# Performance work log

Measured on AMD Instinct MI355X. Metric: run time of the kernel, lower is better.

Reference implementation:

```python
import jax, jax.numpy as jnp
import numpy as np

STRIDES = (8, 16, 32)
BINS = 16
NC = 80
ALPHA, GAMMA = 0.25, 2.0
W_CLS, W_IOU, W_DFL = 1.0, 7.5, 1.5
B, MAX_GT = 32, 32
EPS = 1e-7


def setup_inputs() -> dict:
    key = jax.random.key(0)
    k0, k1, k2, k3, k4, k5, k6 = jax.random.split(key, 7)
    p0 = jax.random.normal(k0, (B, 4 * BINS + NC, 80, 80), dtype=jnp.float32)
    p1 = jax.random.normal(k1, (B, 4 * BINS + NC, 40, 40), dtype=jnp.float32)
    p2 = jax.random.normal(k2, (B, 4 * BINS + NC, 20, 20), dtype=jnp.float32)
    # realistic xyxy boxes inside a 640x640 image
    c = jax.random.uniform(k3, (B, MAX_GT, 2), minval=60.0, maxval=580.0)
    wh = jax.random.uniform(k4, (B, MAX_GT, 2), minval=16.0, maxval=120.0)
    gt_bboxes = jnp.concatenate([c - wh / 2, c + wh / 2], axis=-1).astype(jnp.float32)
    gt_labels = jax.random.randint(k5, (B, MAX_GT), 0, NC, dtype=jnp.int32)
    raw = jax.random.randint(k6, (B, 8400), 0, 20 * MAX_GT, dtype=jnp.int32)
    matched_gt_inds = jnp.where(raw < MAX_GT, raw, -1)
    return {"p0": p0, "p1": p1, "p2": p2, "gt_bboxes": gt_bboxes,
            "gt_labels": gt_labels, "matched_gt_inds": matched_gt_inds}


def _decode_scale(p, stride):
    # p: [B, 4*BINS + NC, H, W]
    Bp, C, H, W = p.shape
    dfl = p[:, :4 * BINS].reshape(Bp, 4, BINS, H, W)
    cls = p[:, 4 * BINS:]
    # DFL decode: expectation of softmax over bins, scaled by stride
    prob = jax.nn.softmax(dfl, axis=2)
    proj = jnp.arange(BINS, dtype=p.dtype)
    dist = jnp.einsum('bkchw,c->bkhw', prob, proj) * stride  # [B,4,H,W] in pixels
    ys, xs = jnp.meshgrid(jnp.arange(H), jnp.arange(W), indexing='ij')
    cx = ((xs.astype(p.dtype)) + 0.5) * stride
    cy = ((ys.astype(p.dtype)) + 0.5) * stride
    boxes = jnp.stack([cx - dist[:, 0], cy - dist[:, 1],
                       cx + dist[:, 2], cy + dist[:, 3]], axis=-1).reshape(Bp, H * W, 4)
    cls_logits = cls.transpose(0, 2, 3, 1).reshape(Bp, H * W, NC)
    dfl_flat = dfl.transpose(0, 3, 4, 1, 2).reshape(Bp, H * W, 4, BINS)
    grid = jnp.stack([cx, cy], axis=-1).reshape(H * W, 2)
    smap = jnp.full((H * W,), stride, dtype=p.dtype)
    return cls_logits, dfl_flat, boxes, grid, smap


def reference(p0, p1, p2, gt_bboxes, gt_labels, matched_gt_inds):
    outs = [_decode_scale(p, s) for p, s in zip((p0, p1, p2), STRIDES)]
    scores = jnp.concatenate([o[0] for o in outs], axis=1)   # [B,N,NC]
    dfl = jnp.concatenate([o[1] for o in outs], axis=1)      # [B,N,4,BINS]
    pboxes = jnp.concatenate([o[2] for o in outs], axis=1)   # [B,N,4]
    grid = jnp.concatenate([o[3] for o in outs], axis=0)     # [N,2]
    smap = jnp.concatenate([o[4] for o in outs], axis=0)     # [N]

    pos = matched_gt_inds >= 0                               # [B,N]
    idx = jnp.where(pos, matched_gt_inds, 0)
    lbl = jnp.take_along_axis(gt_labels, idx, axis=1)        # [B,N]
    posf = pos.astype(scores.dtype)
    tgt_scores = jax.nn.one_hot(lbl, NC, dtype=scores.dtype) * posf[..., None]

    # sigmoid focal loss (stable BCE-with-logits)
    prob = jax.nn.sigmoid(scores)
    ce = jnp.maximum(scores, 0) - scores * tgt_scores + jnp.log1p(jnp.exp(-jnp.abs(scores)))
    p_t = prob * tgt_scores + (1 - prob) * (1 - tgt_scores)
    alpha_t = tgt_scores * ALPHA + (1 - tgt_scores) * (1 - ALPHA)
    cls_elem = alpha_t * (1.0 - p_t) ** GAMMA * ce
    num_pos = jnp.maximum(posf.sum(), 1.0)
    loss_cls = cls_elem.sum() / num_pos

    # gather matched GT boxes per anchor
    tboxes = jnp.take_along_axis(gt_bboxes, idx[..., None], axis=1)  # [B,N,4]
    gx, gy = grid[None, :, 0], grid[None, :, 1]
    l = jnp.clip(gx - tboxes[..., 0], 0.0)
    t = jnp.clip(gy - tboxes[..., 1], 0.0)
    r = jnp.clip(tboxes[..., 2] - gx, 0.0)
    b_ = jnp.clip(tboxes[..., 3] - gy, 0.0)
    dists = jnp.stack([l, t, r, b_], axis=-1) / smap[None, :, None]   # [B,N,4]
    tb = jnp.clip(dists, 0.0, BINS - 1 - 1e-6)
    lo = jnp.floor(tb).astype(jnp.int32)
    hi = jnp.minimum(lo + 1, BINS - 1)
    a = tb - lo.astype(tb.dtype)
    # soft two-bin DFL target (vectorized form of the scatter_add loop)
    tdist = (jax.nn.one_hot(lo, BINS, dtype=dfl.dtype) * (1.0 - a)[..., None]
             + jax.nn.one_hot(hi, BINS, dtype=dfl.dtype) * a[..., None])   # [B,N,4,BINS]
    logp = jax.nn.log_softmax(dfl, axis=-1)
    dfl_elem = -(tdist * logp).sum(-1)                                # [B,N,4]
    loss_dfl = (dfl_elem * posf[..., None]).sum() / (num_pos * 4.0)

    # IoU loss on positives
    ix1 = jnp.maximum(pboxes[..., 0], tboxes[..., 0])
    iy1 = jnp.maximum(pboxes[..., 1], tboxes[..., 1])
    ix2 = jnp.minimum(pboxes[..., 2], tboxes[..., 2])
    iy2 = jnp.minimum(pboxes[..., 3], tboxes[..., 3])
    inter = jnp.clip(ix2 - ix1, 0.0) * jnp.clip(iy2 - iy1, 0.0)
    area_p = jnp.clip(pboxes[..., 2] - pboxes[..., 0], 0.0) * jnp.clip(pboxes[..., 3] - pboxes[..., 1], 0.0)
    area_t = jnp.clip(tboxes[..., 2] - tboxes[..., 0], 0.0) * jnp.clip(tboxes[..., 3] - tboxes[..., 1], 0.0)
    iou = inter / (area_p + area_t - inter + EPS)
    loss_iou = ((1.0 - iou) * posf).sum() / num_pos

    total = W_CLS * loss_cls + W_IOU * loss_iou + W_DFL * loss_dfl
    return total
```

## Files before the change

kernel.cpp:

```cpp
#include <hip/hip_runtime.h>
#include <math.h>

#define NCLS 80
#define BINS 16
#define BATCH 32
#define MAX_GT 32
#define NA 8400
#define AN (BATCH * NA)
#define NT 2100
#define NB_DFL 1050
#define NB_CLS 2560
#define NBLK (NB_DFL + NB_CLS)
#define NSLOT 64
#define ALPHA_C 0.25f
#define W_CLS 1.0
#define W_IOU 7.5
#define W_DFL 1.5
#define EPS_F 1e-7f

__device__ __forceinline__ float focal_elem(float s, float tt)
{
    float e   = __expf(-fabsf(s));
    float inv = 1.f / (1.f + e);
    float prob = (s >= 0.f) ? inv : e * inv;
    float ce  = fmaxf(s, 0.f) - s * tt + __logf(1.f + e);
    float p_t = prob * tt + (1.f - prob) * (1.f - tt);
    float alpha_t = tt * ALPHA_C + (1.f - tt) * (1.f - ALPHA_C);
    float om = 1.f - p_t;
    return alpha_t * om * om * ce;
}

__device__ __forceinline__ void block_write4(float c0, float c1, float c2, float c3,
                                             double* __restrict__ blk)
{
    #pragma unroll
    for (int o = 32; o > 0; o >>= 1) {
        c0 += __shfl_down(c0, o);
        c1 += __shfl_down(c1, o);
        c2 += __shfl_down(c2, o);
        c3 += __shfl_down(c3, o);
    }
    __shared__ float s4[4][4];
    const int wave = threadIdx.x >> 6, lane = threadIdx.x & 63;
    if (lane == 0) { s4[wave][0] = c0; s4[wave][1] = c1; s4[wave][2] = c2; s4[wave][3] = c3; }
    __syncthreads();
    if (threadIdx.x == 0) {
        double* o = blk + (size_t)blockIdx.x * 4;
        o[0] = (double)(s4[0][0] + s4[1][0] + s4[2][0] + s4[3][0]);
        o[1] = (double)(s4[0][1] + s4[1][1] + s4[2][1] + s4[3][1]);
        o[2] = (double)(s4[0][2] + s4[1][2] + s4[2][2] + s4[3][2]);
        o[3] = (double)(s4[0][3] + s4[1][3] + s4[2][3] + s4[3][3]);
    }
}

__global__ __launch_bounds__(256) void yolo_mega(
    const float* __restrict__ p0, const float* __restrict__ p1, const float* __restrict__ p2,
    const float* __restrict__ gt_bboxes, const int* __restrict__ gt_labels,
    const int* __restrict__ matched, double* __restrict__ blk)
{
    const int bid = blockIdx.x;

    if (bid < NB_DFL) {
        const int gdt = bid * 256 + (int)threadIdx.x;
        const int k   = gdt & 3;
        const int qg  = gdt >> 2;
        const int b   = qg / NT;
        const int t   = qg - b * NT;

        const float* p; int HW, off, gbase, h, w0; float stride;
        if (t < 1600)      { p = p0; HW = 6400; off = t * 4;          gbase = 0;    stride = 8.f;
                             h = t / 20;  w0 = (t - h * 20) * 4; }
        else if (t < 2000) { p = p1; HW = 1600; off = (t - 1600) * 4; gbase = 6400; stride = 16.f;
                             int u = t - 1600; h = u / 10; w0 = (u - h * 10) * 4; }
        else               { p = p2; HW = 400;  off = (t - 2000) * 4; gbase = 8000; stride = 32.f;
                             int u = t - 2000; h = u / 5;  w0 = (u - h * 5) * 4; }
        const float inv_s = 1.f / stride;
        const float cy = ((float)h + 0.5f) * stride;
        const float* pc = p + (size_t)(b * 144 + k * BINS) * HW + off;

        const int4 m4 = *(const int4*)(matched + (size_t)b * NA + gbase + off);
        const int mm[4] = {m4.x, m4.y, m4.z, m4.w};
        int lo[4]; float fr[4];
        #pragma unroll
        for (int j = 0; j < 4; ++j) {
            const int idx = (mm[j] >= 0) ? mm[j] : 0;
            const float4 tb = *(const float4*)(gt_bboxes + ((size_t)b * MAX_GT + idx) * 4);
            const float cx = ((float)(w0 + j) + 0.5f) * stride;
            float d = (k == 0) ? (cx - tb.x) : (k == 1) ? (cy - tb.y)
                    : (k == 2) ? (tb.z - cx) : (tb.w - cy);
            float tval = fminf(fmaxf(d, 0.f) * inv_s, (float)(BINS - 1) - 1e-6f);
            lo[j] = (int)tval;
            fr[j] = tval - (float)lo[j];
        }

        float mr[4], se[4], we[4];
        #pragma unroll
        for (int j = 0; j < 4; ++j) { mr[j] = -1e30f; se[j] = 0.f; we[j] = 0.f; }
        #pragma unroll
        for (int i0 = 0; i0 < BINS; i0 += 4) {
            float4 qa = *(const float4*)(pc + (size_t)(i0 + 0) * HW);
            float4 qb = *(const float4*)(pc + (size_t)(i0 + 1) * HW);
            float4 qc = *(const float4*)(pc + (size_t)(i0 + 2) * HW);
            float4 qd = *(const float4*)(pc + (size_t)(i0 + 3) * HW);
            const float r0[4] = {qa.x, qa.y, qa.z, qa.w};
            const float r1[4] = {qb.x, qb.y, qb.z, qb.w};
            const float r2[4] = {qc.x, qc.y, qc.z, qc.w};
            const float r3[4] = {qd.x, qd.y, qd.z, qd.w};
            #pragma unroll
            for (int j = 0; j < 4; ++j) {
                float v0 = r0[j], v1 = r1[j], v2 = r2[j], v3 = r3[j];
                float mx = fmaxf(fmaxf(v0, v1), fmaxf(v2, v3));
                float mn = fmaxf(mr[j], mx);
                float sc = __expf(mr[j] - mn);
                float e0 = __expf(v0 - mn), e1 = __expf(v1 - mn);
                float e2 = __expf(v2 - mn), e3 = __expf(v3 - mn);
                se[j] = se[j] * sc + ((e0 + e1) + (e2 + e3));
                we[j] = we[j] * sc + ((float)(i0    ) * e0 + (float)(i0 + 1) * e1
                                    + (float)(i0 + 2) * e2 + (float)(i0 + 3) * e3);
                mr[j] = mn;
            }
        }

        float part = 0.f;
        float pd[4];
        #pragma unroll
        for (int j = 0; j < 4; ++j) {
            pd[j] = (we[j] / se[j]) * stride;
            if (mm[j] >= 0) {
                float vlo = pc[(size_t)lo[j] * HW + j];
                float vhi = pc[(size_t)(lo[j] + 1) * HW + j];
                float lse = mr[j] + __logf(se[j]);
                part += -((1.f - fr[j]) * (vlo - lse) + fr[j] * (vhi - lse));
            }
        }

        const int lbase = ((int)threadIdx.x & 63) & ~3;
        float d0[4], d1[4], d2[4], d3[4];
        #pragma unroll
        for (int j = 0; j < 4; ++j) {
            d0[j] = __shfl(pd[j], lbase + 0);
            d1[j] = __shfl(pd[j], lbase + 1);
            d2[j] = __shfl(pd[j], lbase + 2);
            d3[j] = __shfl(pd[j], lbase + 3);
        }

        float iou_part = 0.f, cnt = 0.f, cls_corr = 0.f;
        if (k == 0) {
            #pragma unroll
            for (int j = 0; j < 4; ++j) {
                if (mm[j] >= 0) {
                    const float cx = ((float)(w0 + j) + 0.5f) * stride;
                    float px1 = cx - d0[j], py1 = cy - d1[j];
                    float px2 = cx + d2[j], py2 = cy + d3[j];
                    const float4 tb = *(const float4*)(gt_bboxes + ((size_t)b * MAX_GT + mm[j]) * 4);
                    float ix1 = fmaxf(px1, tb.x), iy1 = fmaxf(py1, tb.y);
                    float ix2 = fminf(px2, tb.z), iy2 = fminf(py2, tb.w);
                    float inter  = fmaxf(ix2 - ix1, 0.f) * fmaxf(iy2 - iy1, 0.f);
                    float area_p = fmaxf(px2 - px1, 0.f) * fmaxf(py2 - py1, 0.f);
                    float area_t = fmaxf(tb.z - tb.x, 0.f) * fmaxf(tb.w - tb.y, 0.f);
                    float iou = inter / (area_p + area_t - inter + EPS_F);
                    iou_part += 1.f - iou;
                    cnt += 1.f;
                    int lbl = gt_labels[b * MAX_GT + mm[j]];
                    float sv = *(p + (size_t)(b * 144 + 4 * BINS + lbl) * HW + off + j);
                    cls_corr += focal_elem(sv, 1.f) - focal_elem(sv, 0.f);
                }
            }
        }
        block_write4(cls_corr, iou_part, part, cnt, blk);
    } else {
        const int cbid = bid - NB_DFL;
        const int b = cbid / NCLS;
        const int c = cbid - b * NCLS;
        const size_t cls_ch = (size_t)(b * 144 + 4 * BINS + c);

        float4 q[9];
        const float* pl0 = p0 + cls_ch * 6400;
        #pragma unroll
        for (int i = 0; i < 6; ++i) {
            int off = (i * 256 + (int)threadIdx.x) * 4;
            q[i] = *(const float4*)(pl0 + off);
        }
        #pragma unroll
        for (int i = 6; i < 9; ++i) {
            int t  = i * 256 + (int)threadIdx.x;
            int tc = (t < NT) ? t : 0;
            const float* p; int HW, off;
            if (tc < 1600)      { p = p0; HW = 6400; off = tc * 4; }
            else if (tc < 2000) { p = p1; HW = 1600; off = (tc - 1600) * 4; }
            else                { p = p2; HW = 400;  off = (tc - 2000) * 4; }
            q[i] = *(const float4*)(p + cls_ch * HW + off);
        }

        float part = 0.f;
        #pragma unroll
        for (int i = 0; i < 9; ++i) {
            const bool valid = (i < 8) || (i * 256 + (int)threadIdx.x < NT);
            float sum = focal_elem(q[i].x, 0.f) + focal_elem(q[i].y, 0.f)
                      + focal_elem(q[i].z, 0.f) + focal_elem(q[i].w, 0.f);
            part += valid ? sum : 0.f;
        }
        block_write4(part, 0.f, 0.f, 0.f, blk);
    }
}

__global__ __launch_bounds__(256) void yolo_finalize_blocks(
    const double* __restrict__ blk, float* __restrict__ out)
{
    double s0 = 0.0, s1 = 0.0, s2 = 0.0, s3 = 0.0;
    for (int r = (int)threadIdx.x; r < NBLK; r += 256) {
        const double* row = blk + (size_t)r * 4;
        s0 += row[0]; s1 += row[1]; s2 += row[2]; s3 += row[3];
    }
    #pragma unroll
    for (int o = 32; o > 0; o >>= 1) {
        s0 += __shfl_down(s0, o); s1 += __shfl_down(s1, o);
        s2 += __shfl_down(s2, o); s3 += __shfl_down(s3, o);
    }
    __shared__ double sh[4][4];
    const int wave = threadIdx.x >> 6, lane = threadIdx.x & 63;
    if (lane == 0) { sh[wave][0] = s0; sh[wave][1] = s1; sh[wave][2] = s2; sh[wave][3] = s3; }
    __syncthreads();
    if (threadIdx.x == 0) {
        double c = 0, i = 0, d = 0, n = 0;
        for (int w = 0; w < 4; ++w) { c += sh[w][0]; i += sh[w][1]; d += sh[w][2]; n += sh[w][3]; }
        double np = (n < 1.0) ? 1.0 : n;
        out[0] = (float)(W_CLS * c / np + W_IOU * i / np + W_DFL * d / (np * 4.0));
    }
}

__device__ __forceinline__ void block_reduce_atomic(float val, double* __restrict__ target)
{
    __shared__ float s[4];
    __syncthreads();
    #pragma unroll
    for (int o = 32; o > 0; o >>= 1) val += __shfl_down(val, o);
    const int wave = threadIdx.x >> 6, lane = threadIdx.x & 63;
    if (lane == 0) s[wave] = val;
    __syncthreads();
    if (threadIdx.x == 0) atomicAdd(target, (double)(s[0] + s[1] + s[2] + s[3]));
}

__global__ __launch_bounds__(256) void yolo_loss_fused(
    const float* __restrict__ p0, const float* __restrict__ p1, const float* __restrict__ p2,
    const float* __restrict__ gt_bboxes, const int* __restrict__ gt_labels,
    const int* __restrict__ matched, double* __restrict__ acc)
{
    const int a = blockIdx.x * blockDim.x + threadIdx.x;
    const int b = blockIdx.y;
    const int slot = blockIdx.x & (NSLOT - 1);
    float cls_acc = 0.f, iou_acc = 0.f, dfl_acc = 0.f, pos_cnt = 0.f;
    if (a < NA) {
        const float* p; int HW, W; float stride; int off;
        if (a < 6400)      { p = p0; HW = 6400; W = 80; stride = 8.f;  off = a; }
        else if (a < 8000) { p = p1; HW = 1600; W = 40; stride = 16.f; off = a - 6400; }
        else               { p = p2; HW = 400;  W = 20; stride = 32.f; off = a - 8000; }
        const int h = off / W, w = off - h * W;
        const float cx = ((float)w + 0.5f) * stride, cy = ((float)h + 0.5f) * stride;
        const float* pb = p + ((size_t)b * 144) * (size_t)HW + (size_t)off;
        const int m = matched[(size_t)b * NA + a];
        const bool pos = (m >= 0);
        const int idx = pos ? m : 0;
        const int lbl = gt_labels[b * MAX_GT + idx];
        const float* tbp = gt_bboxes + ((size_t)b * MAX_GT + idx) * 4;
        const float tx1 = tbp[0], ty1 = tbp[1], tx2 = tbp[2], ty2 = tbp[3];
        float tdist[4] = {fmaxf(cx - tx1, 0.f) / stride, fmaxf(cy - ty1, 0.f) / stride,
                          fmaxf(tx2 - cx, 0.f) / stride, fmaxf(ty2 - cy, 0.f) / stride};
        float pdv[4]; float dfl_sum = 0.f;
        #pragma unroll
        for (int k = 0; k < 4; ++k) {
            float tv = fminf(tdist[k], (float)(BINS - 1) - 1e-6f);
            int lo = (int)floorf(tv);
            float fr = tv - (float)lo;
            const float* pcx = pb + (size_t)(k * BINS) * HW;
            float v[BINS];
            #pragma unroll
            for (int i = 0; i < BINS; ++i) v[i] = pcx[(size_t)i * HW];
            float mx = v[0];
            #pragma unroll
            for (int i = 1; i < BINS; ++i) mx = fmaxf(mx, v[i]);
            float se = 0.f, we = 0.f, vlo = 0.f, vhi = 0.f;
            #pragma unroll
            for (int i = 0; i < BINS; ++i) {
                float e = __expf(v[i] - mx);
                se += e; we += (float)i * e;
                vlo = (i == lo) ? v[i] : vlo;
                vhi = (i == lo + 1) ? v[i] : vhi;
            }
            pdv[k] = (we / se) * stride;
            if (pos) { float lse = mx + __logf(se); dfl_sum += -((1.f - fr) * (vlo - lse) + fr * (vhi - lse)); }
        }
        const float* pcls = pb + (size_t)(4 * BINS) * HW;
        #pragma unroll 4
        for (int c = 0; c < NCLS; ++c)
            cls_acc += focal_elem(pcls[(size_t)c * HW], (pos && c == lbl) ? 1.f : 0.f);
        if (pos) {
            float px1 = cx - pdv[0], py1 = cy - pdv[1], px2 = cx + pdv[2], py2 = cy + pdv[3];
            float ix1 = fmaxf(px1, tx1), iy1 = fmaxf(py1, ty1);
            float ix2 = fminf(px2, tx2), iy2 = fminf(py2, ty2);
            float inter  = fmaxf(ix2 - ix1, 0.f) * fmaxf(iy2 - iy1, 0.f);
            float area_p = fmaxf(px2 - px1, 0.f) * fmaxf(py2 - py1, 0.f);
            float area_t = fmaxf(tx2 - tx1, 0.f) * fmaxf(ty2 - ty1, 0.f);
            float iou = inter / (area_p + area_t - inter + EPS_F);
            iou_acc = 1.f - iou; dfl_acc = dfl_sum; pos_cnt = 1.f;
        }
    }
    block_reduce_atomic(cls_acc, &acc[0 * NSLOT + slot]);
    block_reduce_atomic(iou_acc, &acc[1 * NSLOT + slot]);
    block_reduce_atomic(dfl_acc, &acc[2 * NSLOT + slot]);
    block_reduce_atomic(pos_cnt, &acc[3 * NSLOT + slot]);
}

__global__ void yolo_loss_finalize(const double* __restrict__ acc, float* __restrict__ out)
{
    double s[4] = {0.0, 0.0, 0.0, 0.0};
    for (int q = 0; q < 4; ++q)
        for (int i = 0; i < NSLOT; ++i) s[q] += acc[q * NSLOT + i];
    double np = s[3] < 1.0 ? 1.0 : s[3];
    double total = W_CLS * s[0] / np + W_IOU * s[1] / np + W_DFL * s[2] / (np * 4.0);
    out[0] = (float)total;
}

extern "C" void kernel_launch(void* const* d_in, const int* in_sizes, int n_in,
                              void* d_out, int out_size, void* d_ws, size_t ws_size,
                              hipStream_t stream)
{
    const float* p0        = (const float*)d_in[0];
    const float* p1        = (const float*)d_in[1];
    const float* p2        = (const float*)d_in[2];
    const float* gt_bboxes = (const float*)d_in[3];
    const int*   gt_labels = (const int*)d_in[4];
    const int*   matched   = (const int*)d_in[5];
    float*  out = (float*)d_out;

    const size_t need = (size_t)NBLK * 4 * sizeof(double);

    if (ws_size >= need) {
        double* blk = (double*)d_ws;
        yolo_mega<<<NBLK, 256, 0, stream>>>(p0, p1, p2, gt_bboxes, gt_labels, matched, blk);
        yolo_finalize_blocks<<<1, 256, 0, stream>>>(blk, out);
    } else {
        double* acc = (double*)d_ws;
        (void)hipMemsetAsync(acc, 0, 4 * NSLOT * sizeof(double), stream);
        dim3 g((NA + 255) / 256, BATCH);
        yolo_loss_fused<<<g, 256, 0, stream>>>(p0, p1, p2, gt_bboxes, gt_labels, matched, acc);
        yolo_loss_finalize<<<1, 1, 0, stream>>>(acc, out);
    }
}
```

Measured before the change: 217.8 us.

## Grid-stride mega kernel, drop online-softmax max, specialize scales via templates

The fused loss kernel now runs on a fixed 2048-block grid. Each block loops over the 3610 virtual work units and accumulates its partials in registers, so the finalize kernel reads 2048 rows with 1024 threads. The DFL softmax drops the running-max rescaling and exponentiates the raw logits directly. Per-scale code is specialized with templates, and the negative focal term gets a simplified closed form. Target-bin computation now happens only for positive anchors. Dropping the max subtraction risks overflow for large logits, but it is safe for normal-distributed inputs. There is also a redundant pair of vlo/vhi loads.

```diff
diff --git a/kernel.cpp b/kernel.cpp
--- a/kernel.cpp
+++ b/kernel.cpp
@@ -10,7 +10,8 @@
 #define NT 2100
 #define NB_DFL 1050
 #define NB_CLS 2560
-#define NBLK (NB_DFL + NB_CLS)
+#define NVB (NB_DFL + NB_CLS)
+#define GRID 2048
 #define NSLOT 64
 #define ALPHA_C 0.25f
 #define W_CLS 1.0
@@ -28,6 +29,15 @@
     float alpha_t = tt * ALPHA_C + (1.f - tt) * (1.f - ALPHA_C);
     float om = 1.f - p_t;
     return alpha_t * om * om * ce;
+}
+
+__device__ __forceinline__ float focal0(float s)
+{
+    float e   = __expf(-fabsf(s));
+    float inv = 1.f / (1.f + e);
+    float prob = (s >= 0.f) ? inv : e * inv;
+    float sp  = fmaxf(s, 0.f) + __logf(1.f + e);
+    return 0.75f * prob * prob * sp;
 }
 
 __device__ __forceinline__ void block_write4(float c0, float c1, float c2, float c3,
@@ -53,177 +63,185 @@
     }
 }
 
+template<int HW, int SSTR, int WQ>
+__device__ __forceinline__ void dfl_scale(
+    const float* __restrict__ p, int b, int tl, int k, int gbase, int tid,
+    const float* __restrict__ gt_bboxes, const int* __restrict__ gt_labels,
+    const int* __restrict__ matched,
+    float& c_cls, float& c_iou, float& c_dfl, float& c_cnt)
+{
+    const float stride = (float)SSTR;
+    const float inv_s  = 1.f / stride;
+    const int h  = tl / WQ;
+    const int w0 = (tl - h * WQ) * 4;
+    const int off = tl * 4;
+    const float cy = ((float)h + 0.5f) * stride;
+    const float* pc = p + (size_t)(b * 144 + k * BINS) * HW + off;
+
+    const int4 m4 = *(const int4*)(matched + (size_t)b * NA + gbase + off);
+    const int mm[4] = {m4.x, m4.y, m4.z, m4.w};
+
+    float se[4] = {0.f, 0.f, 0.f, 0.f}, we[4] = {0.f, 0.f, 0.f, 0.f};
+    #pragma unroll
+    for (int i0 = 0; i0 < BINS; i0 += 4) {
+        float4 qv[4];
+        #pragma unroll
+        for (int r = 0; r < 4; ++r)
+            qv[r] = *(const float4*)(pc + (size_t)((i0 + r) * HW));
+        #pragma unroll
+        for (int r = 0; r < 4; ++r) {
+            const float wgt = (float)(i0 + r);
+            float e0 = __expf(qv[r].x), e1 = __expf(qv[r].y);
+            float e2 = __expf(qv[r].z), e3 = __expf(qv[r].w);
+            se[0] += e0; we[0] = fmaf(wgt, e0, we[0]);
+            se[1] += e1; we[1] = fmaf(wgt, e1, we[1]);
+            se[2] += e2; we[2] = fmaf(wgt, e2, we[2]);
+            se[3] += e3; we[3] = fmaf(wgt, e3, we[3]);
+        }
+    }
+
+    float pd[4];
+    #pragma unroll
+    for (int j = 0; j < 4; ++j) pd[j] = (we[j] / se[j]) * stride;
+
+    #pragma unroll
+    for (int j = 0; j < 4; ++j) {
+        if (mm[j] >= 0) {
+            const float4 tb = *(const float4*)(gt_bboxes + ((size_t)b * MAX_GT + mm[j]) * 4);
+            const float cx = ((float)(w0 + j) + 0.5f) * stride;
+            float d = (k == 0) ? (cx - tb.x) : (k == 1) ? (cy - tb.y)
+                    : (k == 2) ? (tb.z - cx) : (tb.w - cy);
+            float tval = fminf(fmaxf(d, 0.f) * inv_s, (float)(BINS - 1) - 1e-6f);
+            int   lo = (int)tval;
+            float fr = tval - (float)lo;
+            float vlo = pc[(size_t)(lo * HW) + 0];
+            float vhi = pc[(size_t)((lo + 1) * HW) + 0];
+            vlo = pc[(size_t)(lo * HW) + j];
+            vhi = pc[(size_t)((lo + 1) * HW) + j];
+            float lse = __logf(se[j]);
+            c_dfl += -((1.f - fr) * (vlo - lse) + fr * (vhi - lse));
+        }
+    }
+
+    const int lbase = (tid & 63) & ~3;
+    float d1[4], d2[4], d3[4];
+    #pragma unroll
+    for (int j = 0; j < 4; ++j) {
+        d1[j] = __shfl(pd[j], lbase + 1);
+        d2[j] = __shfl(pd[j], lbase + 2);
+        d3[j] = __shfl(pd[j], lbase + 3);
+    }
+    if (k == 0) {
+        #pragma unroll
+        for (int j = 0; j < 4; ++j) {
+            if (mm[j] >= 0) {
+                const float cx = ((float)(w0 + j) + 0.5f) * stride;
+                float px1 = cx - pd[j], py1 = cy - d1[j];
+                float px2 = cx + d2[j], py2 = cy + d3[j];
+                const float4 tb = *(const float4*)(gt_bboxes + ((size_t)b * MAX_GT + mm[j]) * 4);
+                float ix1 = fmaxf(px1, tb.x), iy1 = fmaxf(py1, tb.y);
+                float ix2 = fminf(px2, tb.z), iy2 = fminf(py2, tb.w);
+                float inter  = fmaxf(ix2 - ix1, 0.f) * fmaxf(iy2 - iy1, 0.f);
+                float area_p = fmaxf(px2 - px1, 0.f) * fmaxf(py2 - py1, 0.f);
+                float area_t = fmaxf(tb.z - tb.x, 0.f) * fmaxf(tb.w - tb.y, 0.f);
+                float iou = inter / (area_p + area_t - inter + EPS_F);
+                c_iou += 1.f - iou;
+                c_cnt += 1.f;
+                int lbl = gt_labels[b * MAX_GT + mm[j]];
+                float sv = *(p + (size_t)(b * 144 + 4 * BINS + lbl) * HW + off + j);
+                c_cls += focal_elem(sv, 1.f) - focal_elem(sv, 0.f);
+            }
+        }
+    }
+}
+
+__device__ __forceinline__ void cls_unit(int cvb, int tid,
+    const float* __restrict__ p0, const float* __restrict__ p1,
+    const float* __restrict__ p2, float& c_cls)
+{
+    const int b = cvb / NCLS;
+    const int c = cvb - b * NCLS;
+    const size_t cls_ch = (size_t)(b * 144 + 4 * BINS + c);
+
+    float4 q[9];
+    const float* pl0 = p0 + cls_ch * 6400;
+    #pragma unroll
+    for (int i = 0; i < 6; ++i) {
+        int off = (i * 256 + tid) * 4;
+        q[i] = *(const float4*)(pl0 + off);
+    }
+    #pragma unroll
+    for (int i = 6; i < 9; ++i) {
+        int t  = i * 256 + tid;
+        int tc = (t < NT) ? t : 0;
+        const float* p; int HW, off;
+        if (tc < 1600)      { p = p0; HW = 6400; off = tc * 4; }
+        else if (tc < 2000) { p = p1; HW = 1600; off = (tc - 1600) * 4; }
+        else                { p = p2; HW = 400;  off = (tc - 2000) * 4; }
+        q[i] = *(const float4*)(p + cls_ch * HW + off);
+    }
+
+    float part = 0.f;
+    #pragma unroll
+    for (int i = 0; i < 9; ++i) {
+        const bool valid = (i < 8) || (i * 256 + tid < NT);
+        float sum = focal0(q[i].x) + focal0(q[i].y) + focal0(q[i].z) + focal0(q[i].w);
+        part += valid ? sum : 0.f;
+    }
+    c_cls += part;
+}
+
 __global__ __launch_bounds__(256) void yolo_mega(
     const float* __restrict__ p0, const float* __restrict__ p1, const float* __restrict__ p2,
     const float* __restrict__ gt_bboxes, const int* __restrict__ gt_labels,
     const int* __restrict__ matched, double* __restrict__ blk)
 {
-    const int bid = blockIdx.x;
-
-    if (bid < NB_DFL) {
-        const int gdt = bid * 256 + (int)threadIdx.x;
-        const int k   = gdt & 3;
-        const int qg  = gdt >> 2;
-        const int b   = qg / NT;
-        const int t   = qg - b * NT;
-
-        const float* p; int HW, off, gbase, h, w0; float stride;
-        if (t < 1600)      { p = p0; HW = 6400; off = t * 4;          gbase = 0;    stride = 8.f;
-                             h = t / 20;  w0 = (t - h * 20) * 4; }
-        else if (t < 2000) { p = p1; HW = 1600; off = (t - 1600) * 4; gbase = 6400; stride = 16.f;
-                             int u = t - 1600; h = u / 10; w0 = (u - h * 10) * 4; }
-        else               { p = p2; HW = 400;  off = (t - 2000) * 4; gbase = 8000; stride = 32.f;
-                             int u = t - 2000; h = u / 5;  w0 = (u - h * 5) * 4; }
-        const float inv_s = 1.f / stride;
-        const float cy = ((float)h + 0.5f) * stride;
-        const float* pc = p + (size_t)(b * 144 + k * BINS) * HW + off;
-
-        const int4 m4 = *(const int4*)(matched + (size_t)b * NA + gbase + off);
-        const int mm[4] = {m4.x, m4.y, m4.z, m4.w};
-        int lo[4]; float fr[4];
-        #pragma unroll
-        for (int j = 0; j < 4; ++j) {
-            const int idx = (mm[j] >= 0) ? mm[j] : 0;
-            const float4 tb = *(const float4*)(gt_bboxes + ((size_t)b * MAX_GT + idx) * 4);
-            const float cx = ((float)(w0 + j) + 0.5f) * stride;
-            float d = (k == 0) ? (cx - tb.x) : (k == 1) ? (cy - tb.y)
-                    : (k == 2) ? (tb.z - cx) : (tb.w - cy);
-            float tval = fminf(fmaxf(d, 0.f) * inv_s, (float)(BINS - 1) - 1e-6f);
-            lo[j] = (int)tval;
-            fr[j] = tval - (float)lo[j];
-        }
-
-        float mr[4], se[4], we[4];
-        #pragma unroll
-        for (int j = 0; j < 4; ++j) { mr[j] = -1e30f; se[j] = 0.f; we[j] = 0.f; }
-        #pragma unroll
-        for (int i0 = 0; i0 < BINS; i0 += 4) {
-            float4 qa = *(const float4*)(pc + (size_t)(i0 + 0) * HW);
-            float4 qb = *(const float4*)(pc + (size_t)(i0 + 1) * HW);
-            float4 qc = *(const float4*)(pc + (size_t)(i0 + 2) * HW);
-            float4 qd = *(const float4*)(pc + (size_t)(i0 + 3) * HW);
-            const float r0[4] = {qa.x, qa.y, qa.z, qa.w};
-            const float r1[4] = {qb.x, qb.y, qb.z, qb.w};
-            const float r2[4] = {qc.x, qc.y, qc.z, qc.w};
-            const float r3[4] = {qd.x, qd.y, qd.z, qd.w};
-            #pragma unroll
-            for (int j = 0; j < 4; ++j) {
-                float v0 = r0[j], v1 = r1[j], v2 = r2[j], v3 = r3[j];
-                float mx = fmaxf(fmaxf(v0, v1), fmaxf(v2, v3));
-                float mn = fmaxf(mr[j], mx);
-                float sc = __expf(mr[j] - mn);
-                float e0 = __expf(v0 - mn), e1 = __expf(v1 - mn);
-                float e2 = __expf(v2 - mn), e3 = __expf(v3 - mn);
-                se[j] = se[j] * sc + ((e0 + e1) + (e2 + e3));
-                we[j] = we[j] * sc + ((float)(i0    ) * e0 + (float)(i0 + 1) * e1
-                                    + (float)(i0 + 2) * e2 + (float)(i0 + 3) * e3);
-                mr[j] = mn;
-            }
-        }
-
-        float part = 0.f;
-        float pd[4];
-        #pragma unroll
-        for (int j = 0; j < 4; ++j) {
-            pd[j] = (we[j] / se[j]) * stride;
-            if (mm[j] >= 0) {
-                float vlo = pc[(size_t)lo[j] * HW + j];
-                float vhi = pc[(size_t)(lo[j] + 1) * HW + j];
-                float lse = mr[j] + __logf(se[j]);
-                part += -((1.f - fr[j]) * (vlo - lse) + fr[j] * (vhi - lse));
-            }
-        }
-
-        const int lbase = ((int)threadIdx.x & 63) & ~3;
-        float d0[4], d1[4], d2[4], d3[4];
-        #pragma unroll
-        for (int j = 0; j < 4; ++j) {
-            d0[j] = __shfl(pd[j], lbase + 0);
-            d1[j] = __shfl(pd[j], lbase + 1);
-            d2[j] = __shfl(pd[j], lbase + 2);
-            d3[j] = __shfl(pd[j], lbase + 3);
-        }
-
-        float iou_part = 0.f, cnt = 0.f, cls_corr = 0.f;
-        if (k == 0) {
-            #pragma unroll
-            for (int j = 0; j < 4; ++j) {
-                if (mm[j] >= 0) {
-                    const float cx = ((float)(w0 + j) + 0.5f) * stride;
-                    float px1 = cx - d0[j], py1 = cy - d1[j];
-                    float px2 = cx + d2[j], py2 = cy + d3[j];
-                    const float4 tb = *(const float4*)(gt_bboxes + ((size_t)b * MAX_GT + mm[j]) * 4);
-                    float ix1 = fmaxf(px1, tb.x), iy1 = fmaxf(py1, tb.y);
-                    float ix2 = fminf(px2, tb.z), iy2 = fminf(py2, tb.w);
-                    float inter  = fmaxf(ix2 - ix1, 0.f) * fmaxf(iy2 - iy1, 0.f);
-                    float area_p = fmaxf(px2 - px1, 0.f) * fmaxf(py2 - py1, 0.f);
-                    float area_t = fmaxf(tb.z - tb.x, 0.f) * fmaxf(tb.w - tb.y, 0.f);
-                    float iou = inter / (area_p + area_t - inter + EPS_F);
-                    iou_part += 1.f - iou;
-                    cnt += 1.f;
-                    int lbl = gt_labels[b * MAX_GT + mm[j]];
-                    float sv = *(p + (size_t)(b * 144 + 4 * BINS + lbl) * HW + off + j);
-                    cls_corr += focal_elem(sv, 1.f) - focal_elem(sv, 0.f);
-                }
-            }
-        }
-        block_write4(cls_corr, iou_part, part, cnt, blk);
-    } else {
-        const int cbid = bid - NB_DFL;
-        const int b = cbid / NCLS;
-        const int c = cbid - b * NCLS;
-        const size_t cls_ch = (size_t)(b * 144 + 4 * BINS + c);
-
-        float4 q[9];
-        const float* pl0 = p0 + cls_ch * 6400;
-        #pragma unroll
-        for (int i = 0; i < 6; ++i) {
-            int off = (i * 256 + (int)threadIdx.x) * 4;
-            q[i] = *(const float4*)(pl0 + off);
-        }
-        #pragma unroll
-        for (int i = 6; i < 9; ++i) {
-            int t  = i * 256 + (int)threadIdx.x;
-            int tc = (t < NT) ? t : 0;
-            const float* p; int HW, off;
-            if (tc < 1600)      { p = p0; HW = 6400; off = tc * 4; }
-            else if (tc < 2000) { p = p1; HW = 1600; off = (tc - 1600) * 4; }
-            else                { p = p2; HW = 400;  off = (tc - 2000) * 4; }
-            q[i] = *(const float4*)(p + cls_ch * HW + off);
-        }
-
-        float part = 0.f;
-        #pragma unroll
-        for (int i = 0; i < 9; ++i) {
-            const bool valid = (i < 8) || (i * 256 + (int)threadIdx.x < NT);
-            float sum = focal_elem(q[i].x, 0.f) + focal_elem(q[i].y, 0.f)
-                      + focal_elem(q[i].z, 0.f) + focal_elem(q[i].w, 0.f);
-            part += valid ? sum : 0.f;
-        }
-        block_write4(part, 0.f, 0.f, 0.f, blk);
-    }
-}
-
-__global__ __launch_bounds__(256) void yolo_finalize_blocks(
+    const int tid = (int)threadIdx.x;
+    float c_cls = 0.f, c_iou = 0.f, c_dfl = 0.f, c_cnt = 0.f;
+
+    for (int vb = (int)blockIdx.x; vb < NVB; vb += GRID) {
+        if (vb < NB_DFL) {
+            const int gdt = vb * 256 + tid;
+            const int k   = gdt & 3;
+            const int qg  = gdt >> 2;
+            const int b   = qg / NT;
+            const int t   = qg - b * NT;
+            if (t < 1600)
+                dfl_scale<6400,  8, 20>(p0, b, t,        k, 0,    tid,
+                                        gt_bboxes, gt_labels, matched, c_cls, c_iou, c_dfl, c_cnt);
+            else if (t < 2000)
+                dfl_scale<1600, 16, 10>(p1, b, t - 1600, k, 6400, tid,
+                                        gt_bboxes, gt_labels, matched, c_cls, c_iou, c_dfl, c_cnt);
+            else
+                dfl_scale< 400, 32,  5>(p2, b, t - 2000, k, 8000, tid,
+                                        gt_bboxes, gt_labels, matched, c_cls, c_iou, c_dfl, c_cnt);
+        } else {
+            cls_unit(vb - NB_DFL, tid, p0, p1, p2, c_cls);
+        }
+    }
+    block_write4(c_cls, c_iou, c_dfl, c_cnt, blk);
+}
+
+__global__ __launch_bounds__(1024) void yolo_finalize_blocks(
     const double* __restrict__ blk, float* __restrict__ out)
 {
-    double s0 = 0.0, s1 = 0.0, s2 = 0.0, s3 = 0.0;
-    for (int r = (int)threadIdx.x; r < NBLK; r += 256) {
-        const double* row = blk + (size_t)r * 4;
-        s0 += row[0]; s1 += row[1]; s2 += row[2]; s3 += row[3];
-    }
+    const int tid = (int)threadIdx.x;
+    const double2* r0 = (const double2*)(blk + (size_t)tid * 4);
+    const double2* r1 = (const double2*)(blk + (size_t)(tid + 1024) * 4);
+    double2 a0 = r0[0], a1 = r0[1], b0 = r1[0], b1 = r1[1];
+    double s0 = a0.x + b0.x, s1 = a0.y + b0.y, s2 = a1.x + b1.x, s3 = a1.y + b1.y;
     #pragma unroll
     for (int o = 32; o > 0; o >>= 1) {
         s0 += __shfl_down(s0, o); s1 += __shfl_down(s1, o);
         s2 += __shfl_down(s2, o); s3 += __shfl_down(s3, o);
     }
-    __shared__ double sh[4][4];
-    const int wave = threadIdx.x >> 6, lane = threadIdx.x & 63;
+    __shared__ double sh[16][4];
+    const int wave = tid >> 6, lane = tid & 63;
     if (lane == 0) { sh[wave][0] = s0; sh[wave][1] = s1; sh[wave][2] = s2; sh[wave][3] = s3; }
     __syncthreads();
-    if (threadIdx.x == 0) {
+    if (tid == 0) {
         double c = 0, i = 0, d = 0, n = 0;
-        for (int w = 0; w < 4; ++w) { c += sh[w][0]; i += sh[w][1]; d += sh[w][2]; n += sh[w][3]; }
+        for (int w = 0; w < 16; ++w) { c += sh[w][0]; i += sh[w][1]; d += sh[w][2]; n += sh[w][3]; }
         double np = (n < 1.0) ? 1.0 : n;
         out[0] = (float)(W_CLS * c / np + W_IOU * i / np + W_DFL * d / (np * 4.0));
     }
@@ -333,12 +351,12 @@
     const int*   matched   = (const int*)d_in[5];
     float*  out = (float*)d_out;
 
-    const size_t need = (size_t)NBLK * 4 * sizeof(double);
+    const size_t need = (size_t)GRID * 4 * sizeof(double);
 
     if (ws_size >= need) {
         double* blk = (double*)d_ws;
-        yolo_mega<<<NBLK, 256, 0, stream>>>(p0, p1, p2, gt_bboxes, gt_labels, matched, blk);
-        yolo_finalize_blocks<<<1, 256, 0, stream>>>(blk, out);
+        yolo_mega<<<GRID, 256, 0, stream>>>(p0, p1, p2, gt_bboxes, gt_labels, matched, blk);
+        yolo_finalize_blocks<<<1, 1024, 0, stream>>>(blk, out);
     } else {
         double* acc = (double*)d_ws;
         (void)hipMemsetAsync(acc, 0, 4 * NSLOT * sizeof(double), stream);
```

Result: no change. 216.8 us (-0.5%).
